# Kernel optimization log

Measured on AMD Instinct MI355X. Metric: run time of the kernel, lower is better.

Reference implementation:

```python
import jax, jax.numpy as jnp
import numpy as np

DIM = 2048
N_HEAD = 32
N_KV_HEAD = 8
HEAD_DIM = DIM // N_HEAD  # 64
BSZ = 2
SEQ = 2048


def apply_rotary_emb(x, freqs_cis):
    # x: [b, s, h, d]; freqs_cis: [s, d//2, 2]
    xs = x.reshape(*x.shape[:-1], -1, 2)          # [b, s, h, d//2, 2]
    fc = freqs_cis.reshape(1, xs.shape[1], 1, xs.shape[3], 2)
    x0, x1 = xs[..., 0], xs[..., 1]
    c, s = fc[..., 0], fc[..., 1]
    out = jnp.stack([x0 * c - x1 * s, x1 * c + x0 * s], axis=-1)
    return out.reshape(x.shape).astype(x.dtype)


def setup_inputs() -> dict:
    key = jax.random.key(0)
    k1, k2, k3, k4 = jax.random.split(key, 4)
    x = jax.random.normal(k1, (BSZ, SEQ, DIM), dtype=jnp.float32)
    # rotary cos/sin table [seq, head_dim//2, 2]
    theta = 1.0 / (10000.0 ** (jnp.arange(0, HEAD_DIM, 2, dtype=jnp.float32) / HEAD_DIM))
    ang = jnp.arange(SEQ, dtype=jnp.float32)[:, None] * theta[None, :]
    freqs_cis = jnp.stack([jnp.cos(ang), jnp.sin(ang)], axis=-1)
    mask = jnp.tril(jnp.ones((SEQ, SEQ), dtype=bool))  # causal
    scale = 0.02
    wqkv = jax.random.normal(k2, ((N_HEAD + 2 * N_KV_HEAD) * HEAD_DIM, DIM), dtype=jnp.float32) * scale
    wo = jax.random.normal(k3, (DIM, DIM), dtype=jnp.float32) * scale
    return {"x": x, "freqs_cis": freqs_cis, "mask": mask, "wqkv": wqkv, "wo": wo}


def reference(x, freqs_cis, mask, wqkv, wo):
    bsz, seqlen, _ = x.shape
    kv_size = N_KV_HEAD * HEAD_DIM
    qkv = x @ wqkv.T  # [b, s, dim + 2*kv]
    xq, xk, xv = jnp.split(qkv, [DIM, DIM + kv_size], axis=-1)
    xq = xq.reshape(bsz, seqlen, N_HEAD, HEAD_DIM)
    xk = xk.reshape(bsz, seqlen, N_KV_HEAD, HEAD_DIM)
    xv = xv.reshape(bsz, seqlen, N_KV_HEAD, HEAD_DIM)
    xq = apply_rotary_emb(xq, freqs_cis)
    xk = apply_rotary_emb(xk, freqs_cis)
    # [b, h, s, d]
    xq = xq.transpose(0, 2, 1, 3)
    xk = xk.transpose(0, 2, 1, 3)
    xv = xv.transpose(0, 2, 1, 3)
    rep = N_HEAD // N_KV_HEAD
    keys = jnp.repeat(xk, rep, axis=1)
    values = jnp.repeat(xv, rep, axis=1)
    scores = jnp.einsum("bhqd,bhkd->bhqk", xq, keys) / np.sqrt(HEAD_DIM).astype(np.float32)
    scores = jnp.where(mask, scores, jnp.finfo(scores.dtype).min)
    attn = jax.nn.softmax(scores, axis=-1)
    out = jnp.einsum("bhqk,bhkd->bhqd", attn, values)
    out = out.transpose(0, 2, 1, 3).reshape(bsz, seqlen, DIM)
    return out @ wo.T
```

## Files before the change

kernel.cpp:

```cpp
#include <hip/hip_runtime.h>
#include <hip/hip_bf16.h>

typedef __attribute__((ext_vector_type(8))) short short8;
typedef __attribute__((ext_vector_type(4))) short short4v;
typedef __attribute__((ext_vector_type(4))) float f32x4;
typedef __hip_bfloat16 bf16;

#define SEQ 2048
#define DIM 2048
#define NH 32
#define NKV 8
#define HD 64
#define QKVD 3072
#define KVD 512

__device__ inline void gld_lds16(const bf16* g, bf16* l) {
    __builtin_amdgcn_global_load_lds((const __attribute__((address_space(1))) void*)g,
                                     (__attribute__((address_space(3))) void*)l, 16, 0, 0);
}

__device__ inline void store_val(float* p, float v) { *p = v; }
__device__ inline void store_val(bf16* p, float v) { *p = __float2bfloat16(v); }

__global__ void cvt_kernel(const float* __restrict__ in, bf16* __restrict__ out, int n4) {
    int i = blockIdx.x * blockDim.x + threadIdx.x;
    if (i < n4) {
        float4 v = ((const float4*)in)[i];
        ushort4 u;
        bf16 b0 = __float2bfloat16(v.x); u.x = *(unsigned short*)&b0;
        bf16 b1 = __float2bfloat16(v.y); u.y = *(unsigned short*)&b1;
        bf16 b2 = __float2bfloat16(v.z); u.z = *(unsigned short*)&b2;
        bf16 b3 = __float2bfloat16(v.w); u.w = *(unsigned short*)&b3;
        ((ushort4*)out)[i] = u;
    }
}

template <typename CT>
__global__ __launch_bounds__(256, 2) void gemm_nt(const bf16* __restrict__ A,
                                                  const bf16* __restrict__ Bt,
                                                  CT* __restrict__ C,
                                                  int M, int N, int K) {
    __shared__ bf16 As[128 * 32];
    __shared__ bf16 Bs[128 * 32];
    const int tid = threadIdx.x;
    const int lane = tid & 63;
    const int quad = lane >> 4;
    const int r16 = lane & 15;
    const int wave = tid >> 6;
    const int bm = blockIdx.y * 128;
    const int bn = blockIdx.x * 128;
    const int wm = (wave >> 1) * 64;
    const int wn = (wave & 1) * 64;

    f32x4 acc[4][4] = {};

    const int arow = tid >> 2;
    const int kch = (tid & 3) * 8;
    const bf16* Ap = A + (size_t)(bm + arow) * K + kch;
    const bf16* Bp = Bt + (size_t)(bn + arow) * K + kch;
    bf16* Asd = As + tid * 8;
    bf16* Bsd = Bs + tid * 8;
    const int kq = quad * 8;

    for (int k0 = 0; k0 < K; k0 += 32) {
        __syncthreads();
        gld_lds16(Ap, Asd);
        gld_lds16(Ap + (size_t)64 * K, Asd + 64 * 32);
        gld_lds16(Bp, Bsd);
        gld_lds16(Bp + (size_t)64 * K, Bsd + 64 * 32);
        Ap += 32; Bp += 32;
        __syncthreads();
        short8 af[4], bfr[4];
#pragma unroll
        for (int i = 0; i < 4; i++)
            af[i] = *(const short8*)(As + (wm + i * 16 + r16) * 32 + kq);
#pragma unroll
        for (int j = 0; j < 4; j++)
            bfr[j] = *(const short8*)(Bs + (wn + j * 16 + r16) * 32 + kq);
#pragma unroll
        for (int i = 0; i < 4; i++)
#pragma unroll
            for (int j = 0; j < 4; j++)
                acc[i][j] = __builtin_amdgcn_mfma_f32_16x16x32_bf16(af[i], bfr[j], acc[i][j], 0, 0, 0);
    }
#pragma unroll
    for (int i = 0; i < 4; i++)
#pragma unroll
        for (int j = 0; j < 4; j++) {
            int row = bm + wm + i * 16 + quad * 4;
            int col = bn + wn + j * 16 + r16;
#pragma unroll
            for (int r = 0; r < 4; r++)
                store_val(C + (size_t)(row + r) * N + col, acc[i][j][r]);
        }
}

__global__ void rope_kernel(const bf16* __restrict__ qkv, const float* __restrict__ fc,
                            bf16* __restrict__ qr, bf16* __restrict__ kr, bf16* __restrict__ vt) {
    int p = blockIdx.x * blockDim.x + threadIdx.x;
    int row = blockIdx.y;
    int s = row & (SEQ - 1);
    int b = row >> 11;
    int col = p * 2;
    const bf16* src = qkv + (size_t)row * QKVD + col;
    float x0 = __bfloat162float(src[0]);
    float x1 = __bfloat162float(src[1]);
    if (col < DIM) {
        int j = (col & 63) >> 1;
        float c = fc[(s * 32 + j) * 2 + 0];
        float sn = fc[(s * 32 + j) * 2 + 1];
        qr[(size_t)row * DIM + col]     = __float2bfloat16(x0 * c - x1 * sn);
        qr[(size_t)row * DIM + col + 1] = __float2bfloat16(x1 * c + x0 * sn);
    } else if (col < DIM + KVD) {
        int ck = col - DIM;
        int j = (ck & 63) >> 1;
        float c = fc[(s * 32 + j) * 2 + 0];
        float sn = fc[(s * 32 + j) * 2 + 1];
        kr[(size_t)row * KVD + ck]     = __float2bfloat16(x0 * c - x1 * sn);
        kr[(size_t)row * KVD + ck + 1] = __float2bfloat16(x1 * c + x0 * sn);
    } else {
        int cv = col - DIM - KVD;
        int kvh = cv >> 6;
        int d = cv & 63;
        size_t base = (((size_t)b * NKV + kvh) * HD + d) * SEQ + s;
        vt[base] = __float2bfloat16(x0);
        vt[base + SEQ] = __float2bfloat16(x1);
    }
}

#define SMSCALE 0.18033688011112042f

__global__ __launch_bounds__(256, 2) void attn_kernel(const bf16* __restrict__ qr,
                                                      const bf16* __restrict__ kr,
                                                      const bf16* __restrict__ vt,
                                                      bf16* __restrict__ out) {
    __shared__ bf16 Ks[8192];
    __shared__ bf16 Vs[8192];
    const int t = threadIdx.x;
    const int lane = t & 63;
    const int wv = t >> 6;
    const int quad = lane >> 4;
    const int r16 = lane & 15;
    const int b = blockIdx.y >> 3;
    const int kvh = blockIdx.y & 7;
    const int qt = (blockIdx.y < 8) ? (31 - (int)blockIdx.x) : (int)blockIdx.x;
    const int q0 = qt * 64;
    const int h = kvh * 4 + wv;
    const int nkb = qt + 1;

    const bf16* Kg = kr + ((size_t)b * SEQ + (t & 63)) * KVD + kvh * HD + (t >> 6) * 8;
    const bf16* Vg = vt + ((size_t)(b * NKV + kvh) * HD + (t & 63)) * SEQ + (t >> 6) * 8;

    const bf16* Qp = qr + ((size_t)b * SEQ + q0 + r16) * DIM + h * HD + quad * 8;
    short8 qa[4][2];
#pragma unroll
    for (int qs = 0; qs < 4; qs++)
#pragma unroll
        for (int c = 0; c < 2; c++)
            qa[qs][c] = *(const short8*)(Qp + (size_t)qs * 16 * DIM + c * 32);

    f32x4 o[4][4] = {};
    float m_i[4], l_i[4];
#pragma unroll
    for (int qs = 0; qs < 4; qs++) { m_i[qs] = -__builtin_inff(); l_i[qs] = 0.f; }

    const char* kl = (const char*)Ks + quad * 1024 + r16 * 16;
    const char* vl = (const char*)Vs + (quad >> 1) * 1024 + r16 * 16 + (quad & 1) * 8;

    {
        bf16* Ksd = Ks + t * 8;
        bf16* Vsd = Vs + t * 8;
        gld_lds16(Kg, Ksd);      gld_lds16(Kg + 32, Ksd + 2048);
        gld_lds16(Vg, Vsd);      gld_lds16(Vg + 32, Vsd + 2048);
    }

    for (int kb = 0; kb < nkb; kb++) {
        __syncthreads();
        const int buf = kb & 1;
        if (kb + 1 < nkb) {
            const bf16* Kgn = Kg + (size_t)(kb + 1) * 64 * KVD;
            const bf16* Vgn = Vg + (kb + 1) * 64;
            bf16* Ksd = Ks + (buf ^ 1) * 4096 + t * 8;
            bf16* Vsd = Vs + (buf ^ 1) * 4096 + t * 8;
            gld_lds16(Kgn, Ksd);      gld_lds16(Kgn + 32, Ksd + 2048);
            gld_lds16(Vgn, Vsd);      gld_lds16(Vgn + 32, Vsd + 2048);
        }
        const char* klb = kl + buf * 8192;
        const char* vlb = vl + buf * 8192;
        const bool diag = (kb == nkb - 1);

#pragma unroll
        for (int half = 0; half < 2; half++) {
            short8 kf[2][2];
#pragma unroll
            for (int n2 = 0; n2 < 2; n2++)
#pragma unroll
                for (int c = 0; c < 2; c++)
                    kf[n2][c] = *(const short8*)(klb + c * 4096 + (half * 2 + n2) * 256);

            const f32x4 z = {0.f, 0.f, 0.f, 0.f};
            f32x4 st[2][4];
#pragma unroll
            for (int n2 = 0; n2 < 2; n2++)
#pragma unroll
                for (int qs = 0; qs < 4; qs++) {
                    st[n2][qs] = __builtin_amdgcn_mfma_f32_16x16x32_bf16(kf[n2][0], qa[qs][0], z, 0, 0, 0);
                    st[n2][qs] = __builtin_amdgcn_mfma_f32_16x16x32_bf16(kf[n2][1], qa[qs][1], st[n2][qs], 0, 0, 0);
                }

            float sv[2][4][4];
#pragma unroll
            for (int n2 = 0; n2 < 2; n2++)
#pragma unroll
                for (int qs = 0; qs < 4; qs++)
#pragma unroll
                    for (int r = 0; r < 4; r++)
                        sv[n2][qs][r] = st[n2][qs][r] * SMSCALE;
            if (diag) {
#pragma unroll
                for (int n2 = 0; n2 < 2; n2++) {
                    const int n = half * 2 + n2;
#pragma unroll
                    for (int qs = 0; qs < 4; qs++) {
                        if (n > qs) {
#pragma unroll
                            for (int r = 0; r < 4; r++) sv[n2][qs][r] = -__builtin_inff();
                        } else if (n == qs) {
#pragma unroll
                            for (int r = 0; r < 4; r++)
                                sv[n2][qs][r] = (quad * 4 + r <= r16) ? sv[n2][qs][r] : -__builtin_inff();
                        }
                    }
                }
            }

            float al[4];
            short4v pbs[4][2];
#pragma unroll
            for (int qs = 0; qs < 4; qs++) {
                float mx = sv[0][qs][0];
#pragma unroll
                for (int n2 = 0; n2 < 2; n2++)
#pragma unroll
                    for (int r = 0; r < 4; r++) mx = fmaxf(mx, sv[n2][qs][r]);
                mx = fmaxf(mx, __shfl_xor(mx, 16, 64));
                mx = fmaxf(mx, __shfl_xor(mx, 32, 64));
                float mn = fmaxf(m_i[qs], mx);
                al[qs] = exp2f(m_i[qs] - mn);
                m_i[qs] = mn;
                float ls = 0.f;
#pragma unroll
                for (int n2 = 0; n2 < 2; n2++)
#pragma unroll
                    for (int r = 0; r < 4; r++) {
                        float p = exp2f(sv[n2][qs][r] - mn);
                        ls += p;
                        bf16 pbf = __float2bfloat16(p);
                        pbs[qs][n2][r] = *(short*)&pbf;
                    }
                ls += __shfl_xor(ls, 16, 64);
                ls += __shfl_xor(ls, 32, 64);
                l_i[qs] = l_i[qs] * al[qs] + ls;
            }

            short4v vf[4][2];
#pragma unroll
            for (int dt = 0; dt < 4; dt++)
#pragma unroll
                for (int n2 = 0; n2 < 2; n2++)
                    vf[dt][n2] = *(const short4v*)(vlb + (half * 2 + n2) * 2048 + dt * 256);

#pragma unroll
            for (int qs = 0; qs < 4; qs++)
#pragma unroll
                for (int dt = 0; dt < 4; dt++) {
#pragma unroll
                    for (int r = 0; r < 4; r++) o[qs][dt][r] *= al[qs];
#pragma unroll
                    for (int n2 = 0; n2 < 2; n2++)
                        o[qs][dt] = __builtin_amdgcn_mfma_f32_16x16x16bf16_1k(vf[dt][n2], pbs[qs][n2], o[qs][dt], 0, 0, 0);
                }
        }
    }

#pragma unroll
    for (int qs = 0; qs < 4; qs++) {
        float inv_l = 1.f / l_i[qs];
        bf16* Op = out + ((size_t)b * SEQ + q0 + qs * 16 + r16) * DIM + h * HD + quad * 4;
#pragma unroll
        for (int dt = 0; dt < 4; dt++) {
            short4v pk;
#pragma unroll
            for (int r = 0; r < 4; r++) {
                bf16 v = __float2bfloat16(o[qs][dt][r] * inv_l);
                pk[r] = *(short*)&v;
            }
            *(short4v*)(Op + dt * 16) = pk;
        }
    }
}

extern "C" void kernel_launch(void* const* d_in, const int* in_sizes, int n_in,
                              void* d_out, int out_size, void* d_ws, size_t ws_size,
                              hipStream_t stream) {
    (void)in_sizes; (void)n_in; (void)out_size; (void)ws_size;
    const float* x    = (const float*)d_in[0];
    const float* fc   = (const float*)d_in[1];
    const float* wqkv = (const float*)d_in[3];
    const float* wo   = (const float*)d_in[4];
    float* out = (float*)d_out;

    char* w = (char*)d_ws;
    bf16* xb    = (bf16*)(w);
    bf16* wqkvb = (bf16*)(w + 16777216);
    bf16* wob   = (bf16*)(w + 29360128);
    bf16* qkvb  = (bf16*)(w + 37748736);
    bf16* kr    = (bf16*)(w + 62914560);
    bf16* vt    = (bf16*)(w + 67108864);
    bf16* qr = xb;
    bf16* attnb = qkvb;

    cvt_kernel<<<8192, 256, 0, stream>>>(x, xb, 2097152);
    cvt_kernel<<<6144, 256, 0, stream>>>(wqkv, wqkvb, 1572864);
    cvt_kernel<<<4096, 256, 0, stream>>>(wo, wob, 1048576);
    gemm_nt<bf16><<<dim3(24, 32), 256, 0, stream>>>(xb, wqkvb, qkvb, 4096, QKVD, DIM);
    rope_kernel<<<dim3(6, 4096), 256, 0, stream>>>(qkvb, fc, qr, kr, vt);
    attn_kernel<<<dim3(32, 16), 256, 0, stream>>>(qr, kr, vt, attnb);
    gemm_nt<float><<<dim3(16, 32), 256, 0, stream>>>(attnb, wob, out, 4096, DIM, DIM);
}
```

Measured before the change: 380.2 us.

## Merge conversions, fold softmax scale into RoPE, pair attention query tiles

Merges the three fp32-to-bf16 conversion launches into one kernel with packed bf16x2 stores. Folds the softmax scale into Q during RoPE, removing the per-score multiply. Restructures attention so each block handles two 32-row query tiles (a short one and its mirror) for causal load balancing, processing all 64 keys per iteration. Also raises the GEMM launch bound to three blocks per SM, which may cause register spills.

```diff
diff --git a/kernel.cpp b/kernel.cpp
--- a/kernel.cpp
+++ b/kernel.cpp
@@ -13,6 +13,7 @@
 #define HD 64
 #define QKVD 3072
 #define KVD 512
+#define SMSCALE 0.18033688011112042f
 
 __device__ inline void gld_lds16(const bf16* g, bf16* l) {
     __builtin_amdgcn_global_load_lds((const __attribute__((address_space(1))) void*)g,
@@ -22,21 +23,27 @@
 __device__ inline void store_val(float* p, float v) { *p = v; }
 __device__ inline void store_val(bf16* p, float v) { *p = __float2bfloat16(v); }
 
-__global__ void cvt_kernel(const float* __restrict__ in, bf16* __restrict__ out, int n4) {
+__device__ inline unsigned pkbf16(float a, float b) {
+    __hip_bfloat162 h = __float22bfloat162_rn(make_float2(a, b));
+    return *(unsigned*)&h;
+}
+
+__global__ void cvt3_kernel(const float* __restrict__ x, const float* __restrict__ wqkv,
+                            const float* __restrict__ wo, bf16* __restrict__ out) {
     int i = blockIdx.x * blockDim.x + threadIdx.x;
-    if (i < n4) {
-        float4 v = ((const float4*)in)[i];
-        ushort4 u;
-        bf16 b0 = __float2bfloat16(v.x); u.x = *(unsigned short*)&b0;
-        bf16 b1 = __float2bfloat16(v.y); u.y = *(unsigned short*)&b1;
-        bf16 b2 = __float2bfloat16(v.z); u.z = *(unsigned short*)&b2;
-        bf16 b3 = __float2bfloat16(v.w); u.w = *(unsigned short*)&b3;
-        ((ushort4*)out)[i] = u;
-    }
+    const float* src; int off;
+    if (i < 2097152) { src = x; off = i; }
+    else if (i < 3670016) { src = wqkv; off = i - 2097152; }
+    else { src = wo; off = i - 3670016; }
+    float4 v = ((const float4*)src)[off];
+    uint2 u;
+    u.x = pkbf16(v.x, v.y);
+    u.y = pkbf16(v.z, v.w);
+    ((uint2*)out)[i] = u;
 }
 
 template <typename CT>
-__global__ __launch_bounds__(256, 2) void gemm_nt(const bf16* __restrict__ A,
+__global__ __launch_bounds__(256, 3) void gemm_nt(const bf16* __restrict__ A,
                                                   const bf16* __restrict__ Bt,
                                                   CT* __restrict__ C,
                                                   int M, int N, int K) {
@@ -109,8 +116,8 @@
         int j = (col & 63) >> 1;
         float c = fc[(s * 32 + j) * 2 + 0];
         float sn = fc[(s * 32 + j) * 2 + 1];
-        qr[(size_t)row * DIM + col]     = __float2bfloat16(x0 * c - x1 * sn);
-        qr[(size_t)row * DIM + col + 1] = __float2bfloat16(x1 * c + x0 * sn);
+        qr[(size_t)row * DIM + col]     = __float2bfloat16((x0 * c - x1 * sn) * SMSCALE);
+        qr[(size_t)row * DIM + col + 1] = __float2bfloat16((x1 * c + x0 * sn) * SMSCALE);
     } else if (col < DIM + KVD) {
         int ck = col - DIM;
         int j = (ck & 63) >> 1;
@@ -128,8 +135,6 @@
     }
 }
 
-#define SMSCALE 0.18033688011112042f
-
 __global__ __launch_bounds__(256, 2) void attn_kernel(const bf16* __restrict__ qr,
                                                       const bf16* __restrict__ kr,
                                                       const bf16* __restrict__ vt,
@@ -143,106 +148,99 @@
     const int r16 = lane & 15;
     const int b = blockIdx.y >> 3;
     const int kvh = blockIdx.y & 7;
-    const int qt = (blockIdx.y < 8) ? (31 - (int)blockIdx.x) : (int)blockIdx.x;
-    const int q0 = qt * 64;
+    const int pairIdx = blockIdx.x;
     const int h = kvh * 4 + wv;
-    const int nkb = qt + 1;
 
     const bf16* Kg = kr + ((size_t)b * SEQ + (t & 63)) * KVD + kvh * HD + (t >> 6) * 8;
     const bf16* Vg = vt + ((size_t)(b * NKV + kvh) * HD + (t & 63)) * SEQ + (t >> 6) * 8;
 
-    const bf16* Qp = qr + ((size_t)b * SEQ + q0 + r16) * DIM + h * HD + quad * 8;
-    short8 qa[4][2];
-#pragma unroll
-    for (int qs = 0; qs < 4; qs++)
-#pragma unroll
-        for (int c = 0; c < 2; c++)
-            qa[qs][c] = *(const short8*)(Qp + (size_t)qs * 16 * DIM + c * 32);
-
-    f32x4 o[4][4] = {};
-    float m_i[4], l_i[4];
-#pragma unroll
-    for (int qs = 0; qs < 4; qs++) { m_i[qs] = -__builtin_inff(); l_i[qs] = 0.f; }
-
     const char* kl = (const char*)Ks + quad * 1024 + r16 * 16;
     const char* vl = (const char*)Vs + (quad >> 1) * 1024 + r16 * 16 + (quad & 1) * 8;
 
-    {
-        bf16* Ksd = Ks + t * 8;
-        bf16* Vsd = Vs + t * 8;
-        gld_lds16(Kg, Ksd);      gld_lds16(Kg + 32, Ksd + 2048);
-        gld_lds16(Vg, Vsd);      gld_lds16(Vg + 32, Vsd + 2048);
-    }
-
-    for (int kb = 0; kb < nkb; kb++) {
+    union PB { short4v s; unsigned u[2]; };
+
+#pragma unroll 1
+    for (int seg = 0; seg < 2; seg++) {
+        const int qt = seg ? (63 - pairIdx) : pairIdx;
+        const int q0 = qt * 32;
+        const int nkb = (qt >> 1) + 1;
+
+        const bf16* Qp = qr + ((size_t)b * SEQ + q0 + r16) * DIM + h * HD + quad * 8;
+        short8 qa[2][2];
+#pragma unroll
+        for (int qs = 0; qs < 2; qs++)
+#pragma unroll
+            for (int c = 0; c < 2; c++)
+                qa[qs][c] = *(const short8*)(Qp + (size_t)qs * 16 * DIM + c * 32);
+
+        f32x4 o[2][4] = {};
+        float m_i[2] = {-__builtin_inff(), -__builtin_inff()};
+        float l_i[2] = {0.f, 0.f};
+
         __syncthreads();
-        const int buf = kb & 1;
-        if (kb + 1 < nkb) {
-            const bf16* Kgn = Kg + (size_t)(kb + 1) * 64 * KVD;
-            const bf16* Vgn = Vg + (kb + 1) * 64;
-            bf16* Ksd = Ks + (buf ^ 1) * 4096 + t * 8;
-            bf16* Vsd = Vs + (buf ^ 1) * 4096 + t * 8;
-            gld_lds16(Kgn, Ksd);      gld_lds16(Kgn + 32, Ksd + 2048);
-            gld_lds16(Vgn, Vsd);      gld_lds16(Vgn + 32, Vsd + 2048);
+        {
+            bf16* Ksd = Ks + t * 8;
+            bf16* Vsd = Vs + t * 8;
+            gld_lds16(Kg, Ksd);      gld_lds16(Kg + 32, Ksd + 2048);
+            gld_lds16(Vg, Vsd);      gld_lds16(Vg + 32, Vsd + 2048);
         }
-        const char* klb = kl + buf * 8192;
-        const char* vlb = vl + buf * 8192;
-        const bool diag = (kb == nkb - 1);
-
-#pragma unroll
-        for (int half = 0; half < 2; half++) {
-            short8 kf[2][2];
-#pragma unroll
-            for (int n2 = 0; n2 < 2; n2++)
-#pragma unroll
-                for (int c = 0; c < 2; c++)
-                    kf[n2][c] = *(const short8*)(klb + c * 4096 + (half * 2 + n2) * 256);
+
+        for (int kb = 0; kb < nkb; kb++) {
+            __syncthreads();
+            const int buf = kb & 1;
+            if (kb + 1 < nkb) {
+                const bf16* Kgn = Kg + (size_t)(kb + 1) * 64 * KVD;
+                const bf16* Vgn = Vg + (kb + 1) * 64;
+                bf16* Ksd = Ks + (buf ^ 1) * 4096 + t * 8;
+                bf16* Vsd = Vs + (buf ^ 1) * 4096 + t * 8;
+                gld_lds16(Kgn, Ksd);      gld_lds16(Kgn + 32, Ksd + 2048);
+                gld_lds16(Vgn, Vsd);      gld_lds16(Vgn + 32, Vsd + 2048);
+            }
+            const char* klb = kl + buf * 8192;
+            const char* vlb = vl + buf * 8192;
 
             const f32x4 z = {0.f, 0.f, 0.f, 0.f};
-            f32x4 st[2][4];
-#pragma unroll
-            for (int n2 = 0; n2 < 2; n2++)
-#pragma unroll
-                for (int qs = 0; qs < 4; qs++) {
-                    st[n2][qs] = __builtin_amdgcn_mfma_f32_16x16x32_bf16(kf[n2][0], qa[qs][0], z, 0, 0, 0);
-                    st[n2][qs] = __builtin_amdgcn_mfma_f32_16x16x32_bf16(kf[n2][1], qa[qs][1], st[n2][qs], 0, 0, 0);
+            f32x4 st[4][2];
+#pragma unroll
+            for (int n = 0; n < 4; n++) {
+                short8 kf0 = *(const short8*)(klb + n * 256);
+                short8 kf1 = *(const short8*)(klb + 4096 + n * 256);
+#pragma unroll
+                for (int qs = 0; qs < 2; qs++) {
+                    st[n][qs] = __builtin_amdgcn_mfma_f32_16x16x32_bf16(kf0, qa[qs][0], z, 0, 0, 0);
+                    st[n][qs] = __builtin_amdgcn_mfma_f32_16x16x32_bf16(kf1, qa[qs][1], st[n][qs], 0, 0, 0);
                 }
-
-            float sv[2][4][4];
-#pragma unroll
-            for (int n2 = 0; n2 < 2; n2++)
-#pragma unroll
-                for (int qs = 0; qs < 4; qs++)
-#pragma unroll
-                    for (int r = 0; r < 4; r++)
-                        sv[n2][qs][r] = st[n2][qs][r] * SMSCALE;
-            if (diag) {
-#pragma unroll
-                for (int n2 = 0; n2 < 2; n2++) {
-                    const int n = half * 2 + n2;
-#pragma unroll
-                    for (int qs = 0; qs < 4; qs++) {
-                        if (n > qs) {
-#pragma unroll
-                            for (int r = 0; r < 4; r++) sv[n2][qs][r] = -__builtin_inff();
-                        } else if (n == qs) {
-#pragma unroll
-                            for (int r = 0; r < 4; r++)
-                                sv[n2][qs][r] = (quad * 4 + r <= r16) ? sv[n2][qs][r] : -__builtin_inff();
+            }
+            short4v vf[4][4];
+#pragma unroll
+            for (int dt = 0; dt < 4; dt++)
+#pragma unroll
+                for (int n = 0; n < 4; n++)
+                    vf[dt][n] = *(const short4v*)(vlb + n * 2048 + dt * 256);
+
+            if (kb == nkb - 1) {
+                const int kbase = kb * 64;
+#pragma unroll
+                for (int n = 0; n < 4; n++)
+#pragma unroll
+                    for (int qs = 0; qs < 2; qs++)
+#pragma unroll
+                        for (int r = 0; r < 4; r++) {
+                            int key = kbase + n * 16 + quad * 4 + r;
+                            int row = q0 + qs * 16 + r16;
+                            if (key > row) st[n][qs][r] = -__builtin_inff();
                         }
-                    }
-                }
-            }
-
-            float al[4];
-            short4v pbs[4][2];
-#pragma unroll
-            for (int qs = 0; qs < 4; qs++) {
-                float mx = sv[0][qs][0];
-#pragma unroll
-                for (int n2 = 0; n2 < 2; n2++)
-#pragma unroll
-                    for (int r = 0; r < 4; r++) mx = fmaxf(mx, sv[n2][qs][r]);
+            }
+
+            float al[2];
+            PB pbs[2][4];
+#pragma unroll
+            for (int qs = 0; qs < 2; qs++) {
+                float mx = st[0][qs][0];
+#pragma unroll
+                for (int n = 0; n < 4; n++)
+#pragma unroll
+                    for (int r = 0; r < 4; r++) mx = fmaxf(mx, st[n][qs][r]);
                 mx = fmaxf(mx, __shfl_xor(mx, 16, 64));
                 mx = fmaxf(mx, __shfl_xor(mx, 32, 64));
                 float mn = fmaxf(m_i[qs], mx);
@@ -250,52 +248,43 @@
                 m_i[qs] = mn;
                 float ls = 0.f;
 #pragma unroll
-                for (int n2 = 0; n2 < 2; n2++)
-#pragma unroll
-                    for (int r = 0; r < 4; r++) {
-                        float p = exp2f(sv[n2][qs][r] - mn);
-                        ls += p;
-                        bf16 pbf = __float2bfloat16(p);
-                        pbs[qs][n2][r] = *(short*)&pbf;
-                    }
+                for (int n = 0; n < 4; n++) {
+                    float p0 = exp2f(st[n][qs][0] - mn);
+                    float p1 = exp2f(st[n][qs][1] - mn);
+                    float p2 = exp2f(st[n][qs][2] - mn);
+                    float p3 = exp2f(st[n][qs][3] - mn);
+                    ls += (p0 + p1) + (p2 + p3);
+                    pbs[qs][n].u[0] = pkbf16(p0, p1);
+                    pbs[qs][n].u[1] = pkbf16(p2, p3);
+                }
                 ls += __shfl_xor(ls, 16, 64);
                 ls += __shfl_xor(ls, 32, 64);
                 l_i[qs] = l_i[qs] * al[qs] + ls;
             }
 
-            short4v vf[4][2];
-#pragma unroll
-            for (int dt = 0; dt < 4; dt++)
-#pragma unroll
-                for (int n2 = 0; n2 < 2; n2++)
-                    vf[dt][n2] = *(const short4v*)(vlb + (half * 2 + n2) * 2048 + dt * 256);
-
-#pragma unroll
-            for (int qs = 0; qs < 4; qs++)
+#pragma unroll
+            for (int qs = 0; qs < 2; qs++)
 #pragma unroll
                 for (int dt = 0; dt < 4; dt++) {
 #pragma unroll
                     for (int r = 0; r < 4; r++) o[qs][dt][r] *= al[qs];
 #pragma unroll
-                    for (int n2 = 0; n2 < 2; n2++)
-                        o[qs][dt] = __builtin_amdgcn_mfma_f32_16x16x16bf16_1k(vf[dt][n2], pbs[qs][n2], o[qs][dt], 0, 0, 0);
+                    for (int n = 0; n < 4; n++)
+                        o[qs][dt] = __builtin_amdgcn_mfma_f32_16x16x16bf16_1k(vf[dt][n], pbs[qs][n].s, o[qs][dt], 0, 0, 0);
                 }
         }
-    }
-
-#pragma unroll
-    for (int qs = 0; qs < 4; qs++) {
-        float inv_l = 1.f / l_i[qs];
-        bf16* Op = out + ((size_t)b * SEQ + q0 + qs * 16 + r16) * DIM + h * HD + quad * 4;
-#pragma unroll
-        for (int dt = 0; dt < 4; dt++) {
-            short4v pk;
-#pragma unroll
-            for (int r = 0; r < 4; r++) {
-                bf16 v = __float2bfloat16(o[qs][dt][r] * inv_l);
-                pk[r] = *(short*)&v;
-            }
-            *(short4v*)(Op + dt * 16) = pk;
+
+#pragma unroll
+        for (int qs = 0; qs < 2; qs++) {
+            float inv_l = 1.f / l_i[qs];
+            bf16* Op = out + ((size_t)b * SEQ + q0 + qs * 16 + r16) * DIM + h * HD + quad * 4;
+#pragma unroll
+            for (int dt = 0; dt < 4; dt++) {
+                PB pk;
+                pk.u[0] = pkbf16(o[qs][dt][0] * inv_l, o[qs][dt][1] * inv_l);
+                pk.u[1] = pkbf16(o[qs][dt][2] * inv_l, o[qs][dt][3] * inv_l);
+                *(short4v*)(Op + dt * 16) = pk.s;
+            }
         }
     }
 }
@@ -320,9 +309,7 @@
     bf16* qr = xb;
     bf16* attnb = qkvb;
 
-    cvt_kernel<<<8192, 256, 0, stream>>>(x, xb, 2097152);
-    cvt_kernel<<<6144, 256, 0, stream>>>(wqkv, wqkvb, 1572864);
-    cvt_kernel<<<4096, 256, 0, stream>>>(wo, wob, 1048576);
+    cvt3_kernel<<<18432, 256, 0, stream>>>(x, wqkv, wo, xb);
     gemm_nt<bf16><<<dim3(24, 32), 256, 0, stream>>>(xb, wqkvb, qkvb, 4096, QKVD, DIM);
     rope_kernel<<<dim3(6, 4096), 256, 0, stream>>>(qkvb, fc, qr, kr, vt);
     attn_kernel<<<dim3(32, 16), 256, 0, stream>>>(qr, kr, vt, attnb);
```

After: 352.1 us. 1.08x faster.
